# Performance work log

Measured on AMD Instinct MI355X. Metric: run time of the kernel, lower is better.

The kernel has to match this reference:

```python
import jax, jax.numpy as jnp
import numpy as np

C_Z = 128
N_HEADS = 4
HEAD_DIM = 32
TOTAL = N_HEADS * HEAD_DIM
B, N = 1, 256


def setup_inputs() -> dict:
    key = jax.random.key(0)
    ks = jax.random.split(key, 10)
    s = lambda k, sh: jax.random.normal(k, sh, dtype=jnp.float32) * 0.02
    return {
        "pair_representation": jax.random.normal(ks[0], (B, N, N, C_Z), dtype=jnp.float32),
        "ln_gamma": jnp.ones((C_Z,), jnp.float32),
        "ln_beta": jnp.zeros((C_Z,), jnp.float32),
        "Wq": s(ks[1], (C_Z, TOTAL)),
        "Wk": s(ks[2], (C_Z, TOTAL)),
        "Wv": s(ks[3], (C_Z, TOTAL)),
        "Wb": s(ks[4], (C_Z, N_HEADS)),
        "Wg": s(ks[5], (C_Z, TOTAL)),
        "bg": jnp.zeros((TOTAL,), jnp.float32),
        "Wo": s(ks[6], (TOTAL, C_Z)),
        "bo": jnp.zeros((C_Z,), jnp.float32),
    }


def reference(pair_representation, ln_gamma, ln_beta, Wq, Wk, Wv, Wb, Wg, bg, Wo, bo):
    x = pair_representation
    # LayerNorm over c_z
    mu = jnp.mean(x, axis=-1, keepdims=True)
    var = jnp.mean((x - mu) ** 2, axis=-1, keepdims=True)
    x = (x - mu) * jax.lax.rsqrt(var + 1e-5) * ln_gamma + ln_beta

    b, n, _, _ = x.shape
    split = lambda t: t.reshape(b, n, n, N_HEADS, HEAD_DIM)
    Q = split(x @ Wq)  # [b,i,j,h,d]
    K = split(x @ Wk)
    V = split(x @ Wv)
    G = jax.nn.sigmoid(split(x @ Wg + bg))
    Bias = x @ Wb  # [b,j,k,h]

    scores = jnp.einsum("bijhd,bikhd->bijkh", Q, K) / np.float32(np.sqrt(HEAD_DIM))
    scores = scores + Bias[:, None]  # broadcast over i
    attn = jax.nn.softmax(scores, axis=3)  # over k
    vals = jnp.einsum("bijkh,bikhd->bijhd", attn, V)
    vals = (G * vals).reshape(b, n, n, TOTAL)
    return vals @ Wo + bo
```

## Files before the change

kernel.cpp:

```cpp
#include <hip/hip_runtime.h>
#include <hip/hip_bf16.h>


#define QSCALE 0.17677669529663687f

typedef __attribute__((ext_vector_type(8))) short bf16x8;
typedef __attribute__((ext_vector_type(4))) float f32x4;

__device__ __forceinline__ ushort f2bf(float f) {
    uint32_t u = __builtin_bit_cast(uint32_t, f);
    uint32_t r = (u + 0x7FFFu + ((u >> 16) & 1u)) >> 16;
    return (ushort)r;
}
__device__ __forceinline__ float bf2f(ushort b) {
    return __builtin_bit_cast(float, ((uint32_t)b) << 16);
}
__device__ __forceinline__ uint pk2(float a, float b) {
    union { __hip_bfloat162 h; uint u; } cv;
    cv.h = __float22bfloat162_rn(make_float2(a, b));
    return cv.u;
}
__device__ __forceinline__ float4 ld4f(const float* p) { return *(const float4*)p; }

__global__ __launch_bounds__(256) void prep_kernel(
    const float* __restrict__ Wq, const float* __restrict__ Wk, const float* __restrict__ Wv,
    const float* __restrict__ Wb, const float* __restrict__ Wg, const float* __restrict__ Wo,
    ushort* __restrict__ Wfrag, ushort* __restrict__ WoFrag)
{
    int idx = blockIdx.x * 256 + threadIdx.x;
    if (idx < 67584) {
        int j = idx & 7, lane = (idx >> 3) & 63, ks = (idx >> 9) & 3, ct = idx >> 11;
        int n = ct * 16 + (lane & 15);
        int k = ks * 32 + (lane >> 4) * 8 + j;
        float v = 0.f;
        if (n < 128)      v = Wq[k * 128 + n] * QSCALE;
        else if (n < 256) v = Wk[k * 128 + (n - 128)];
        else if (n < 384) v = Wv[k * 128 + (n - 256)];
        else if (n < 512) v = Wg[k * 128 + (n - 384)];
        else if (n < 516) v = Wb[k * 4 + (n - 512)];
        Wfrag[idx] = f2bf(v);
    } else {
        int idx2 = idx - 67584;
        int j = idx2 & 7, lane = (idx2 >> 3) & 63, ks = (idx2 >> 9) & 3, ct = idx2 >> 11;
        int n = ct * 16 + (lane & 15);
        int k = ks * 32 + (lane >> 4) * 8 + j;
        WoFrag[idx2] = f2bf(Wo[k * 128 + n]);
    }
}

__global__ __launch_bounds__(256) void proj_kernel(
    const float* __restrict__ x, const float* __restrict__ gamma, const float* __restrict__ beta,
    const ushort* __restrict__ Wfrag, const float* __restrict__ bg,
    ushort* __restrict__ Qg, ushort* __restrict__ Kg, ushort* __restrict__ Vtg,
    ushort* __restrict__ Gg, float* __restrict__ BbF)
{
    __shared__ ushort Bs[11 * 2048];
    const int t = threadIdx.x;
    const int wave = t >> 6, lane = t & 63, m = lane & 15, quad = lane >> 4;
    const int p0 = blockIdx.x * 64;
    const int arow = p0 + wave * 16 + m;

    float4 xa[4][2];
    float sum = 0.f, ssq = 0.f;
#pragma unroll
    for (int ks = 0; ks < 4; ++ks) {
        const float* rp = x + arow * 128 + ks * 32 + quad * 8;
        xa[ks][0] = ld4f(rp);
        xa[ks][1] = ld4f(rp + 4);
#pragma unroll
        for (int q4 = 0; q4 < 2; ++q4) {
            float4 v = xa[ks][q4];
            sum += v.x + v.y + v.z + v.w;
            ssq += v.x * v.x + v.y * v.y + v.z * v.z + v.w * v.w;
        }
    }
    sum += __shfl_xor(sum, 16); ssq += __shfl_xor(ssq, 16);
    sum += __shfl_xor(sum, 32); ssq += __shfl_xor(ssq, 32);
    const float mu   = sum * (1.f / 128.f);
    const float var  = ssq * (1.f / 128.f) - mu * mu;
    const float rstd = rsqrtf(var + 1e-5f);

    bf16x8 xf[4];
#pragma unroll
    for (int ks = 0; ks < 4; ++ks) {
        union { bf16x8 v; uint u[4]; } xu;
#pragma unroll
        for (int q4 = 0; q4 < 2; ++q4) {
            const int c = ks * 32 + quad * 8 + q4 * 4;
            float4 g4 = ld4f(gamma + c);
            float4 b4 = ld4f(beta + c);
            float4 v = xa[ks][q4];
            float n0 = (v.x - mu) * rstd * g4.x + b4.x;
            float n1 = (v.y - mu) * rstd * g4.y + b4.y;
            float n2 = (v.z - mu) * rstd * g4.z + b4.z;
            float n3 = (v.w - mu) * rstd * g4.w + b4.w;
            xu.u[q4 * 2]     = pk2(n0, n1);
            xu.u[q4 * 2 + 1] = pk2(n2, n3);
        }
        xf[ks] = xu.v;
    }

    const int p = arow;
    const int i = p >> 8, j2 = p & 255;

    for (int phase = 0; phase < 3; ++phase) {
        const int ctbase = phase * 11;
        __syncthreads();
        const uint4* src = (const uint4*)(Wfrag + ctbase * 2048);
        uint4* dst = (uint4*)Bs;
#pragma unroll
        for (int r = 0; r < 11; ++r) dst[r * 256 + t] = src[r * 256 + t];
        __syncthreads();

        for (int ctl = 0; ctl < 11; ++ctl) {
            const int ct = ctbase + ctl;
            f32x4 acc = (f32x4){0.f, 0.f, 0.f, 0.f};
#pragma unroll
            for (int ks = 0; ks < 4; ++ks) {
                bf16x8 wfr = ((const bf16x8*)Bs)[(ctl * 4 + ks) * 64 + lane];
                acc = __builtin_amdgcn_mfma_f32_16x16x32_bf16(wfr, xf[ks], acc, 0, 0, 0);
            }
            if (ct < 32) {
                const int cls = ct >> 3;
                const int npb = (ct & 7) * 16 + quad * 4;
                const int hh = npb >> 5, d0 = npb & 31;
                if (cls == 2) {
                    const int vb = ((i * 4 + hh) * 32 + d0) * 256 + j2;
#pragma unroll
                    for (int r = 0; r < 4; ++r)
                        Vtg[vb + r * 256] = f2bf(acc[r]);
                } else {
                    const int off = ((i * 4 + hh) * 256 + j2) * 32 + d0;
                    uint2 u;
                    if (cls == 3) {
                        float4 bg4 = ld4f(&bg[npb]);
                        float z0 = 1.f / (1.f + __expf(-(acc[0] + bg4.x)));
                        float z1 = 1.f / (1.f + __expf(-(acc[1] + bg4.y)));
                        float z2 = 1.f / (1.f + __expf(-(acc[2] + bg4.z)));
                        float z3 = 1.f / (1.f + __expf(-(acc[3] + bg4.w)));
                        u.x = pk2(z0, z1); u.y = pk2(z2, z3);
                        *(uint2*)(&Gg[off]) = u;
                    } else {
                        u.x = pk2(acc[0], acc[1]); u.y = pk2(acc[2], acc[3]);
                        if (cls == 0) *(uint2*)(&Qg[off]) = u;
                        else          *(uint2*)(&Kg[off]) = u;
                    }
                }
            } else if (quad == 0) {
#pragma unroll
                for (int r = 0; r < 4; ++r) {
                    int addr = (((r * 16 + (i >> 4)) * 16 + (j2 >> 4)) * 64 +
                                ((j2 & 15) >> 2) * 16 + (i & 15)) * 4 + (j2 & 3);
                    BbF[addr] = acc[r];
                }
            }
        }
    }
}

__global__ __launch_bounds__(256) void attn_kernel(
    const ushort* __restrict__ Qg, const ushort* __restrict__ Kg, const ushort* __restrict__ Vtg,
    const ushort* __restrict__ Gg, const float* __restrict__ BbF, ushort* __restrict__ gvals)
{
    __shared__ ushort Pl[4][64 * 72];
    const int t = threadIdx.x;
    const int wave = t >> 6, lane = t & 63, m = lane & 15, quad = lane >> 4;
    const int ih = blockIdx.x, i = ih >> 2, h = ih & 3;

    const int j0 = wave * 64;
    bf16x8 qf[4];
#pragma unroll
    for (int jt = 0; jt < 4; ++jt)
        qf[jt] = *(const bf16x8*)(Qg + ih * 8192 + (j0 + jt * 16 + m) * 32 + quad * 8);

    f32x4 O[4][2];
    float lsum[4];
#pragma unroll
    for (int jt = 0; jt < 4; ++jt) {
        O[jt][0] = (f32x4){0.f, 0.f, 0.f, 0.f};
        O[jt][1] = (f32x4){0.f, 0.f, 0.f, 0.f};
        lsum[jt] = 0.f;
    }

    for (int kt2 = 0; kt2 < 4; ++kt2) {
        const int k0 = kt2 * 64;
        bf16x8 kf[4];
#pragma unroll
        for (int kk = 0; kk < 4; ++kk)
            kf[kk] = *(const bf16x8*)(Kg + ih * 8192 + (k0 + kk * 16 + m) * 32 + quad * 8);

#pragma unroll
        for (int jt = 0; jt < 4; ++jt) {
            const int jtg = wave * 4 + jt;
#pragma unroll
            for (int kk = 0; kk < 4; ++kk) {
                const int ktg = kt2 * 4 + kk;
                f32x4 bias = *(const f32x4*)(BbF + (((h * 16 + jtg) * 16 + ktg) * 64 + lane) * 4);
                f32x4 S = __builtin_amdgcn_mfma_f32_16x16x32_bf16(kf[kk], qf[jt], bias, 0, 0, 0);
                float pv0 = __expf(S[0]);
                float pv1 = __expf(S[1]);
                float pv2 = __expf(S[2]);
                float pv3 = __expf(S[3]);
                lsum[jt] += pv0 + pv1 + pv2 + pv3;
                uint2 u; u.x = pk2(pv0, pv1); u.y = pk2(pv2, pv3);
                *(uint2*)(&Pl[wave][(jt * 16 + m) * 72 + kk * 16 + quad * 4]) = u;
            }
        }
#pragma unroll
        for (int kc = 0; kc < 2; ++kc) {
            bf16x8 pf[4], vf[2];
#pragma unroll
            for (int jt = 0; jt < 4; ++jt)
                pf[jt] = *(const bf16x8*)(&Pl[wave][(jt * 16 + m) * 72 + kc * 32 + quad * 8]);
#pragma unroll
            for (int dt = 0; dt < 2; ++dt)
                vf[dt] = *(const bf16x8*)(Vtg + (ih * 32 + dt * 16 + m) * 256 + k0 + kc * 32 + quad * 8);
#pragma unroll
            for (int jt = 0; jt < 4; ++jt)
#pragma unroll
                for (int dt = 0; dt < 2; ++dt)
                    O[jt][dt] = __builtin_amdgcn_mfma_f32_16x16x32_bf16(
                        vf[dt], pf[jt], O[jt][dt], 0, 0, 0);
        }
    }

#pragma unroll
    for (int jt = 0; jt < 4; ++jt) {
        float s = lsum[jt];
        s += __shfl_xor(s, 16);
        s += __shfl_xor(s, 32);
        lsum[jt] = 1.f / s;
    }

#pragma unroll
    for (int jt = 0; jt < 4; ++jt) {
        const int j = j0 + jt * 16 + m;
        const float rl = lsum[jt];
#pragma unroll
        for (int dt = 0; dt < 2; ++dt) {
            const int d0 = dt * 16 + quad * 4;
            ushort4 gv = *(const ushort4*)(&Gg[ih * 8192 + j * 32 + d0]);
            float v0 = O[jt][dt][0] * rl * bf2f(gv.x);
            float v1 = O[jt][dt][1] * rl * bf2f(gv.y);
            float v2 = O[jt][dt][2] * rl * bf2f(gv.z);
            float v3 = O[jt][dt][3] * rl * bf2f(gv.w);
            uint2 u; u.x = pk2(v0, v1); u.y = pk2(v2, v3);
            *(uint2*)(&gvals[(i * 256 + j) * 128 + h * 32 + d0]) = u;
        }
    }
}

__global__ __launch_bounds__(256) void oproj_kernel(
    const ushort* __restrict__ gvals, const ushort* __restrict__ WoFrag,
    const float* __restrict__ bo, float* __restrict__ out)
{
    __shared__ ushort Bs[8 * 2048];
    const int t = threadIdx.x;
    const int wave = t >> 6, lane = t & 63, m = lane & 15, quad = lane >> 4;
    const int p0 = blockIdx.x * 64;
    {
        const uint4* src = (const uint4*)WoFrag;
        uint4* dst = (uint4*)Bs;
#pragma unroll
        for (int r = 0; r < 8; ++r) dst[r * 256 + t] = src[r * 256 + t];
    }
    bf16x8 gf[4];
    const int p = p0 + wave * 16 + m;
#pragma unroll
    for (int ks = 0; ks < 4; ++ks)
        gf[ks] = *(const bf16x8*)(gvals + p * 128 + ks * 32 + quad * 8);
    __syncthreads();

#pragma unroll
    for (int ct = 0; ct < 8; ++ct) {
        f32x4 acc = (f32x4){0.f, 0.f, 0.f, 0.f};
#pragma unroll
        for (int ks = 0; ks < 4; ++ks) {
            bf16x8 wfr = ((const bf16x8*)Bs)[(ct * 4 + ks) * 64 + lane];
            acc = __builtin_amdgcn_mfma_f32_16x16x32_bf16(wfr, gf[ks], acc, 0, 0, 0);
        }
        const int c0 = ct * 16 + quad * 4;
        float4 bov = ld4f(&bo[c0]);
        float4 v = make_float4(acc[0] + bov.x, acc[1] + bov.y,
                               acc[2] + bov.z, acc[3] + bov.w);
        *(float4*)(&out[p * 128 + c0]) = v;
    }
}

extern "C" void kernel_launch(void* const* d_in, const int* in_sizes, int n_in,
                              void* d_out, int out_size, void* d_ws, size_t ws_size,
                              hipStream_t stream) {
    const float* x     = (const float*)d_in[0];
    const float* gamma = (const float*)d_in[1];
    const float* beta  = (const float*)d_in[2];
    const float* Wq    = (const float*)d_in[3];
    const float* Wk    = (const float*)d_in[4];
    const float* Wv    = (const float*)d_in[5];
    const float* Wb    = (const float*)d_in[6];
    const float* Wg    = (const float*)d_in[7];
    const float* bg    = (const float*)d_in[8];
    const float* Wo    = (const float*)d_in[9];
    const float* bo    = (const float*)d_in[10];

    ushort* ws     = (ushort*)d_ws;
    ushort* Wfrag  = ws;
    ushort* WoFrag = Wfrag + 67584;
    ushort* Qg     = WoFrag + 16384;
    ushort* Kg     = Qg + 8388608;
    ushort* Vtg    = Kg + 8388608;
    ushort* Gg     = Vtg + 8388608;
    ushort* gvals  = Gg + 8388608;
    float*  BbF    = (float*)(gvals + 8388608);

    prep_kernel<<<328, 256, 0, stream>>>(Wq, Wk, Wv, Wb, Wg, Wo, Wfrag, WoFrag);
    proj_kernel<<<1024, 256, 0, stream>>>(x, gamma, beta, Wfrag, bg, Qg, Kg, Vtg, Gg, BbF);
    attn_kernel<<<1024, 256, 0, stream>>>(Qg, Kg, Vtg, Gg, BbF, gvals);
    oproj_kernel<<<1024, 256, 0, stream>>>(gvals, WoFrag, bo, (float*)d_out);
}
```

Before: 173.4 us.

## Fuse Q/K/V/G projections into attention kernel, precompute LayerNorm and bias

The LayerNorm output is now written once as bf16, and the pair bias is computed in a combined prep kernel. The separate projection and attention kernels are merged into one fused kernel per (i, head). It computes Q, K and V^T into shared memory, runs the attention with 16-wide k steps using 16x16x16 MFMA for PV, and recomputes the gate in the epilogue. This removes the large global round-trips for Q, K, Vt and G, in exchange for redundant projection work per head block and more LDS and register pressure.

New measurement: 172.6 us. About the same (-0.5%).

```diff
diff --git a/kernel.cpp b/kernel.cpp
--- a/kernel.cpp
+++ b/kernel.cpp
@@ -5,173 +5,239 @@
 #define QSCALE 0.17677669529663687f
 
 typedef __attribute__((ext_vector_type(8))) short bf16x8;
+typedef __attribute__((ext_vector_type(4))) short bf16x4;
 typedef __attribute__((ext_vector_type(4))) float f32x4;
+
+#define MFMA32(a, b, c) __builtin_amdgcn_mfma_f32_16x16x32_bf16((a), (b), (c), 0, 0, 0)
+
+__device__ __forceinline__ f32x4 mfma16_asm(bf16x4 a, bf16x4 b, f32x4 c) {
+    f32x4 d;
+    asm volatile("v_mfma_f32_16x16x16_bf16 %0, %1, %2, %3"
+                 : "=v"(d) : "v"(a), "v"(b), "v"(c));
+    return d;
+}
+
+#if !defined(__HIP_DEVICE_COMPILE__)
+#define MFMA16(a, b, c) (c)
+#elif __has_builtin(__builtin_amdgcn_mfma_f32_16x16x16bf16_1k)
+#define MFMA16(a, b, c) __builtin_amdgcn_mfma_f32_16x16x16bf16_1k((a), (b), (c), 0, 0, 0)
+#else
+#define MFMA16(a, b, c) mfma16_asm((a), (b), (c))
+#endif
 
 __device__ __forceinline__ ushort f2bf(float f) {
     uint32_t u = __builtin_bit_cast(uint32_t, f);
     uint32_t r = (u + 0x7FFFu + ((u >> 16) & 1u)) >> 16;
     return (ushort)r;
 }
-__device__ __forceinline__ float bf2f(ushort b) {
-    return __builtin_bit_cast(float, ((uint32_t)b) << 16);
-}
 __device__ __forceinline__ uint pk2(float a, float b) {
     union { __hip_bfloat162 h; uint u; } cv;
     cv.h = __float22bfloat162_rn(make_float2(a, b));
     return cv.u;
 }
-__device__ __forceinline__ float4 ld4f(const float* p) { return *(const float4*)p; }
-
-__global__ __launch_bounds__(256) void prep_kernel(
+
+__global__ __launch_bounds__(256) void prep_bias_kernel(
     const float* __restrict__ Wq, const float* __restrict__ Wk, const float* __restrict__ Wv,
-    const float* __restrict__ Wb, const float* __restrict__ Wg, const float* __restrict__ Wo,
-    ushort* __restrict__ Wfrag, ushort* __restrict__ WoFrag)
+    const float* __restrict__ Wg, const float* __restrict__ Wo, const float* __restrict__ Wb,
+    const float* __restrict__ x, const float* __restrict__ gamma, const float* __restrict__ beta,
+    ushort* __restrict__ Wfrag, ushort* __restrict__ WoFrag,
+    ushort* __restrict__ xn, float* __restrict__ BbF)
 {
-    int idx = blockIdx.x * 256 + threadIdx.x;
-    if (idx < 67584) {
-        int j = idx & 7, lane = (idx >> 3) & 63, ks = (idx >> 9) & 3, ct = idx >> 11;
-        int n = ct * 16 + (lane & 15);
-        int k = ks * 32 + (lane >> 4) * 8 + j;
-        float v = 0.f;
-        if (n < 128)      v = Wq[k * 128 + n] * QSCALE;
-        else if (n < 256) v = Wk[k * 128 + (n - 128)];
-        else if (n < 384) v = Wv[k * 128 + (n - 256)];
-        else if (n < 512) v = Wg[k * 128 + (n - 384)];
-        else if (n < 516) v = Wb[k * 4 + (n - 512)];
-        Wfrag[idx] = f2bf(v);
-    } else {
-        int idx2 = idx - 67584;
-        int j = idx2 & 7, lane = (idx2 >> 3) & 63, ks = (idx2 >> 9) & 3, ct = idx2 >> 11;
-        int n = ct * 16 + (lane & 15);
-        int k = ks * 32 + (lane >> 4) * 8 + j;
-        WoFrag[idx2] = f2bf(Wo[k * 128 + n]);
-    }
-}
-
-__global__ __launch_bounds__(256) void proj_kernel(
-    const float* __restrict__ x, const float* __restrict__ gamma, const float* __restrict__ beta,
-    const ushort* __restrict__ Wfrag, const float* __restrict__ bg,
-    ushort* __restrict__ Qg, ushort* __restrict__ Kg, ushort* __restrict__ Vtg,
-    ushort* __restrict__ Gg, float* __restrict__ BbF)
-{
-    __shared__ ushort Bs[11 * 2048];
+    __shared__ float WbS[512];
+    __shared__ float gS[128];
+    __shared__ float bS[128];
+
+    if (blockIdx.x < 320) {
+        int idx = blockIdx.x * 256 + threadIdx.x;
+        if (idx < 65536) {
+            int j = idx & 7, lane = (idx >> 3) & 63, ks = (idx >> 9) & 3, ct = idx >> 11;
+            int n = ct * 16 + (lane & 15);
+            int k = ks * 32 + (lane >> 4) * 8 + j;
+            float v;
+            if (n < 128)      v = Wq[k * 128 + n] * QSCALE;
+            else if (n < 256) v = Wk[k * 128 + (n - 128)];
+            else if (n < 384) v = Wv[k * 128 + (n - 256)];
+            else              v = Wg[k * 128 + (n - 384)];
+            Wfrag[idx] = f2bf(v);
+        } else {
+            int idx2 = idx - 65536;
+            int j = idx2 & 7, lane = (idx2 >> 3) & 63, ks = (idx2 >> 9) & 3, ct = idx2 >> 11;
+            int n = ct * 16 + (lane & 15);
+            int k = ks * 32 + (lane >> 4) * 8 + j;
+            WoFrag[idx2] = f2bf(Wo[k * 128 + n]);
+        }
+        return;
+    }
+
     const int t = threadIdx.x;
+    if (t < 128)      { *(f32x4*)&WbS[t * 4] = *(const f32x4*)(Wb + t * 4); }
+    else if (t < 160) { int c = (t - 128) * 4; *(f32x4*)&gS[c] = *(const f32x4*)(gamma + c); }
+    else if (t < 192) { int c = (t - 160) * 4; *(f32x4*)&bS[c] = *(const f32x4*)(beta + c); }
+    __syncthreads();
+
     const int wave = t >> 6, lane = t & 63, m = lane & 15, quad = lane >> 4;
-    const int p0 = blockIdx.x * 64;
-    const int arow = p0 + wave * 16 + m;
-
-    float4 xa[4][2];
+    const int p = (blockIdx.x - 320) * 64 + wave * 16 + m;
+
+    const float* rp0 = x + (size_t)p * 128;
+    f32x4 xa[4][2];
     float sum = 0.f, ssq = 0.f;
 #pragma unroll
     for (int ks = 0; ks < 4; ++ks) {
-        const float* rp = x + arow * 128 + ks * 32 + quad * 8;
-        xa[ks][0] = ld4f(rp);
-        xa[ks][1] = ld4f(rp + 4);
+        xa[ks][0] = *(const f32x4*)(rp0 + ks * 32 + quad * 8);
+        xa[ks][1] = *(const f32x4*)(rp0 + ks * 32 + quad * 8 + 4);
 #pragma unroll
         for (int q4 = 0; q4 < 2; ++q4) {
-            float4 v = xa[ks][q4];
-            sum += v.x + v.y + v.z + v.w;
-            ssq += v.x * v.x + v.y * v.y + v.z * v.z + v.w * v.w;
+            f32x4 v = xa[ks][q4];
+            sum += v[0] + v[1] + v[2] + v[3];
+            ssq += v[0]*v[0] + v[1]*v[1] + v[2]*v[2] + v[3]*v[3];
         }
     }
     sum += __shfl_xor(sum, 16); ssq += __shfl_xor(ssq, 16);
     sum += __shfl_xor(sum, 32); ssq += __shfl_xor(ssq, 32);
     const float mu   = sum * (1.f / 128.f);
-    const float var  = ssq * (1.f / 128.f) - mu * mu;
-    const float rstd = rsqrtf(var + 1e-5f);
-
-    bf16x8 xf[4];
+    const float rstd = rsqrtf(ssq * (1.f / 128.f) - mu * mu + 1e-5f);
+
+    float b0 = 0.f, b1 = 0.f, b2 = 0.f, b3 = 0.f;
 #pragma unroll
     for (int ks = 0; ks < 4; ++ks) {
-        union { bf16x8 v; uint u[4]; } xu;
+        uint4 pkd;
+        uint pw[4];
 #pragma unroll
         for (int q4 = 0; q4 < 2; ++q4) {
             const int c = ks * 32 + quad * 8 + q4 * 4;
-            float4 g4 = ld4f(gamma + c);
-            float4 b4 = ld4f(beta + c);
-            float4 v = xa[ks][q4];
-            float n0 = (v.x - mu) * rstd * g4.x + b4.x;
-            float n1 = (v.y - mu) * rstd * g4.y + b4.y;
-            float n2 = (v.z - mu) * rstd * g4.z + b4.z;
-            float n3 = (v.w - mu) * rstd * g4.w + b4.w;
-            xu.u[q4 * 2]     = pk2(n0, n1);
-            xu.u[q4 * 2 + 1] = pk2(n2, n3);
-        }
-        xf[ks] = xu.v;
-    }
-
-    const int p = arow;
-    const int i = p >> 8, j2 = p & 255;
-
-    for (int phase = 0; phase < 3; ++phase) {
-        const int ctbase = phase * 11;
-        __syncthreads();
-        const uint4* src = (const uint4*)(Wfrag + ctbase * 2048);
-        uint4* dst = (uint4*)Bs;
-#pragma unroll
-        for (int r = 0; r < 11; ++r) dst[r * 256 + t] = src[r * 256 + t];
-        __syncthreads();
-
-        for (int ctl = 0; ctl < 11; ++ctl) {
-            const int ct = ctbase + ctl;
-            f32x4 acc = (f32x4){0.f, 0.f, 0.f, 0.f};
-#pragma unroll
-            for (int ks = 0; ks < 4; ++ks) {
-                bf16x8 wfr = ((const bf16x8*)Bs)[(ctl * 4 + ks) * 64 + lane];
-                acc = __builtin_amdgcn_mfma_f32_16x16x32_bf16(wfr, xf[ks], acc, 0, 0, 0);
+            f32x4 v = xa[ks][q4];
+            float n0 = (v[0] - mu) * rstd * gS[c + 0] + bS[c + 0];
+            float n1 = (v[1] - mu) * rstd * gS[c + 1] + bS[c + 1];
+            float n2 = (v[2] - mu) * rstd * gS[c + 2] + bS[c + 2];
+            float n3 = (v[3] - mu) * rstd * gS[c + 3] + bS[c + 3];
+            pw[q4 * 2]     = pk2(n0, n1);
+            pw[q4 * 2 + 1] = pk2(n2, n3);
+            f32x4 w0 = *(const f32x4*)&WbS[(c + 0) * 4];
+            f32x4 w1 = *(const f32x4*)&WbS[(c + 1) * 4];
+            f32x4 w2 = *(const f32x4*)&WbS[(c + 2) * 4];
+            f32x4 w3 = *(const f32x4*)&WbS[(c + 3) * 4];
+            b0 += n0*w0[0] + n1*w1[0] + n2*w2[0] + n3*w3[0];
+            b1 += n0*w0[1] + n1*w1[1] + n2*w2[1] + n3*w3[1];
+            b2 += n0*w0[2] + n1*w1[2] + n2*w2[2] + n3*w3[2];
+            b3 += n0*w0[3] + n1*w1[3] + n2*w2[3] + n3*w3[3];
+        }
+        pkd.x = pw[0]; pkd.y = pw[1]; pkd.z = pw[2]; pkd.w = pw[3];
+        *(uint4*)(xn + (size_t)p * 128 + ks * 32 + quad * 8) = pkd;
+    }
+    b0 += __shfl_xor(b0, 16); b1 += __shfl_xor(b1, 16); b2 += __shfl_xor(b2, 16); b3 += __shfl_xor(b3, 16);
+    b0 += __shfl_xor(b0, 32); b1 += __shfl_xor(b1, 32); b2 += __shfl_xor(b2, 32); b3 += __shfl_xor(b3, 32);
+
+    if (quad == 0) {
+        const int row = p >> 8, col = p & 255;
+        float bb[4] = {b0, b1, b2, b3};
+#pragma unroll
+        for (int r = 0; r < 4; ++r) {
+            int addr = (((r * 16 + (row >> 4)) * 16 + (col >> 4)) * 64 +
+                        ((col & 15) >> 2) * 16 + (row & 15)) * 4 + (col & 3);
+            BbF[addr] = bb[r];
+        }
+    }
+}
+
+__global__ __launch_bounds__(256, 4) void fused_kernel(
+    const ushort* __restrict__ xn, const ushort* __restrict__ Wfrag,
+    const float* __restrict__ bg, const float* __restrict__ BbF,
+    ushort* __restrict__ gvals)
+{
+    __shared__ __align__(16) ushort SM[18688];
+    ushort* QK = SM;
+    ushort* VT = SM + 10240;
+
+    const int t = threadIdx.x;
+    const int w = t >> 6, lane = t & 63, m = lane & 15, quad = lane >> 4;
+    const int i = blockIdx.x >> 2, h = blockIdx.x & 3;
+    const ushort* xb = xn + ((size_t)i << 15);
+
+    {
+        const ushort* Wm = Wfrag + (0 + h * 2) * 2048;
+        bf16x8 wfr[2][4];
+#pragma unroll
+        for (int ctl = 0; ctl < 2; ++ctl)
+#pragma unroll
+            for (int ks = 0; ks < 4; ++ks)
+                wfr[ctl][ks] = *(const bf16x8*)(Wm + ctl * 2048 + ks * 512 + lane * 8);
+#pragma unroll
+        for (int grp = 0; grp < 4; ++grp) {
+            const int j = w * 64 + grp * 16 + m;
+            bf16x8 xg[4];
+            const ushort* xp = xb + (size_t)j * 128 + quad * 8;
+#pragma unroll
+            for (int ks = 0; ks < 4; ++ks) xg[ks] = *(const bf16x8*)(xp + ks * 32);
+#pragma unroll
+            for (int ctl = 0; ctl < 2; ++ctl) {
+                f32x4 acc = (f32x4){0.f, 0.f, 0.f, 0.f};
+#pragma unroll
+                for (int ks = 0; ks < 4; ++ks) acc = MFMA32(wfr[ctl][ks], xg[ks], acc);
+                uint2 u; u.x = pk2(acc[0], acc[1]); u.y = pk2(acc[2], acc[3]);
+                *(uint2*)(QK + j * 40 + ctl * 16 + quad * 4) = u;
             }
-            if (ct < 32) {
-                const int cls = ct >> 3;
-                const int npb = (ct & 7) * 16 + quad * 4;
-                const int hh = npb >> 5, d0 = npb & 31;
-                if (cls == 2) {
-                    const int vb = ((i * 4 + hh) * 32 + d0) * 256 + j2;
-#pragma unroll
-                    for (int r = 0; r < 4; ++r)
-                        Vtg[vb + r * 256] = f2bf(acc[r]);
-                } else {
-                    const int off = ((i * 4 + hh) * 256 + j2) * 32 + d0;
-                    uint2 u;
-                    if (cls == 3) {
-                        float4 bg4 = ld4f(&bg[npb]);
-                        float z0 = 1.f / (1.f + __expf(-(acc[0] + bg4.x)));
-                        float z1 = 1.f / (1.f + __expf(-(acc[1] + bg4.y)));
-                        float z2 = 1.f / (1.f + __expf(-(acc[2] + bg4.z)));
-                        float z3 = 1.f / (1.f + __expf(-(acc[3] + bg4.w)));
-                        u.x = pk2(z0, z1); u.y = pk2(z2, z3);
-                        *(uint2*)(&Gg[off]) = u;
-                    } else {
-                        u.x = pk2(acc[0], acc[1]); u.y = pk2(acc[2], acc[3]);
-                        if (cls == 0) *(uint2*)(&Qg[off]) = u;
-                        else          *(uint2*)(&Kg[off]) = u;
-                    }
-                }
-            } else if (quad == 0) {
-#pragma unroll
-                for (int r = 0; r < 4; ++r) {
-                    int addr = (((r * 16 + (i >> 4)) * 16 + (j2 >> 4)) * 64 +
-                                ((j2 & 15) >> 2) * 16 + (i & 15)) * 4 + (j2 & 3);
-                    BbF[addr] = acc[r];
-                }
+        }
+    }
+    bf16x8 qf[4];
+#pragma unroll
+    for (int jt = 0; jt < 4; ++jt)
+        qf[jt] = *(const bf16x8*)(QK + (w * 64 + jt * 16 + m) * 40 + quad * 8);
+    asm volatile("" ::: "memory");
+
+    {
+        const ushort* Wm = Wfrag + (8 + h * 2) * 2048;
+        bf16x8 wfr[2][4];
+#pragma unroll
+        for (int ctl = 0; ctl < 2; ++ctl)
+#pragma unroll
+            for (int ks = 0; ks < 4; ++ks)
+                wfr[ctl][ks] = *(const bf16x8*)(Wm + ctl * 2048 + ks * 512 + lane * 8);
+#pragma unroll
+        for (int grp = 0; grp < 4; ++grp) {
+            const int k = w * 64 + grp * 16 + m;
+            bf16x8 xg[4];
+            const ushort* xp = xb + (size_t)k * 128 + quad * 8;
+#pragma unroll
+            for (int ks = 0; ks < 4; ++ks) xg[ks] = *(const bf16x8*)(xp + ks * 32);
+#pragma unroll
+            for (int ctl = 0; ctl < 2; ++ctl) {
+                f32x4 acc = (f32x4){0.f, 0.f, 0.f, 0.f};
+#pragma unroll
+                for (int ks = 0; ks < 4; ++ks) acc = MFMA32(wfr[ctl][ks], xg[ks], acc);
+                uint2 u; u.x = pk2(acc[0], acc[1]); u.y = pk2(acc[2], acc[3]);
+                *(uint2*)(QK + k * 40 + ctl * 16 + quad * 4) = u;
             }
         }
     }
-}
-
-__global__ __launch_bounds__(256) void attn_kernel(
-    const ushort* __restrict__ Qg, const ushort* __restrict__ Kg, const ushort* __restrict__ Vtg,
-    const ushort* __restrict__ Gg, const float* __restrict__ BbF, ushort* __restrict__ gvals)
-{
-    __shared__ ushort Pl[4][64 * 72];
-    const int t = threadIdx.x;
-    const int wave = t >> 6, lane = t & 63, m = lane & 15, quad = lane >> 4;
-    const int ih = blockIdx.x, i = ih >> 2, h = ih & 3;
-
-    const int j0 = wave * 64;
-    bf16x8 qf[4];
-#pragma unroll
-    for (int jt = 0; jt < 4; ++jt)
-        qf[jt] = *(const bf16x8*)(Qg + ih * 8192 + (j0 + jt * 16 + m) * 32 + quad * 8);
+    asm volatile("" ::: "memory");
+
+    {
+        const ushort* Wm = Wfrag + (16 + h * 2) * 2048;
+        bf16x8 wfr[2][4];
+#pragma unroll
+        for (int ctl = 0; ctl < 2; ++ctl)
+#pragma unroll
+            for (int ks = 0; ks < 4; ++ks)
+                wfr[ctl][ks] = *(const bf16x8*)(Wm + ctl * 2048 + ks * 512 + lane * 8);
+#pragma unroll
+        for (int grp = 0; grp < 4; ++grp) {
+            const int k = w * 64 + grp * 16 + m;
+            bf16x8 xg[4];
+            const ushort* xp = xb + (size_t)k * 128 + quad * 8;
+#pragma unroll
+            for (int ks = 0; ks < 4; ++ks) xg[ks] = *(const bf16x8*)(xp + ks * 32);
+#pragma unroll
+            for (int ctl = 0; ctl < 2; ++ctl) {
+                f32x4 acc = (f32x4){0.f, 0.f, 0.f, 0.f};
+#pragma unroll
+                for (int ks = 0; ks < 4; ++ks) acc = MFMA32(wfr[ctl][ks], xg[ks], acc);
+#pragma unroll
+                for (int r = 0; r < 4; ++r)
+                    VT[(ctl * 16 + quad * 4 + r) * 264 + k] = f2bf(acc[r]);
+            }
+        }
+    }
+    __syncthreads();
 
     f32x4 O[4][2];
     float lsum[4];
@@ -181,46 +247,28 @@
         O[jt][1] = (f32x4){0.f, 0.f, 0.f, 0.f};
         lsum[jt] = 0.f;
     }
-
-    for (int kt2 = 0; kt2 < 4; ++kt2) {
-        const int k0 = kt2 * 64;
-        bf16x8 kf[4];
-#pragma unroll
-        for (int kk = 0; kk < 4; ++kk)
-            kf[kk] = *(const bf16x8*)(Kg + ih * 8192 + (k0 + kk * 16 + m) * 32 + quad * 8);
-
+    const float* bb = BbF + ((size_t)(h * 16 + w * 4) << 12) + (lane << 2);
+
+    for (int kh = 0; kh < 16; ++kh) {
+        bf16x8 kf = *(const bf16x8*)(QK + (kh * 16 + m) * 40 + quad * 8);
+        bf16x4 vf[2];
+#pragma unroll
+        for (int dt = 0; dt < 2; ++dt) {
+            uint2 vv = *(const uint2*)(VT + (dt * 16 + m) * 264 + kh * 16 + quad * 4);
+            vf[dt] = __builtin_bit_cast(bf16x4, vv);
+        }
 #pragma unroll
         for (int jt = 0; jt < 4; ++jt) {
-            const int jtg = wave * 4 + jt;
-#pragma unroll
-            for (int kk = 0; kk < 4; ++kk) {
-                const int ktg = kt2 * 4 + kk;
-                f32x4 bias = *(const f32x4*)(BbF + (((h * 16 + jtg) * 16 + ktg) * 64 + lane) * 4);
-                f32x4 S = __builtin_amdgcn_mfma_f32_16x16x32_bf16(kf[kk], qf[jt], bias, 0, 0, 0);
-                float pv0 = __expf(S[0]);
-                float pv1 = __expf(S[1]);
-                float pv2 = __expf(S[2]);
-                float pv3 = __expf(S[3]);
-                lsum[jt] += pv0 + pv1 + pv2 + pv3;
-                uint2 u; u.x = pk2(pv0, pv1); u.y = pk2(pv2, pv3);
-                *(uint2*)(&Pl[wave][(jt * 16 + m) * 72 + kk * 16 + quad * 4]) = u;
-            }
-        }
-#pragma unroll
-        for (int kc = 0; kc < 2; ++kc) {
-            bf16x8 pf[4], vf[2];
-#pragma unroll
-            for (int jt = 0; jt < 4; ++jt)
-                pf[jt] = *(const bf16x8*)(&Pl[wave][(jt * 16 + m) * 72 + kc * 32 + quad * 8]);
+            f32x4 S = *(const f32x4*)(bb + (jt << 12) + (kh << 8));
+            S = MFMA32(kf, qf[jt], S);
+            float p0 = __expf(S[0]), p1 = __expf(S[1]);
+            float p2 = __expf(S[2]), p3 = __expf(S[3]);
+            lsum[jt] += p0 + p1 + p2 + p3;
+            uint2 pu; pu.x = pk2(p0, p1); pu.y = pk2(p2, p3);
+            bf16x4 pf = __builtin_bit_cast(bf16x4, pu);
 #pragma unroll
             for (int dt = 0; dt < 2; ++dt)
-                vf[dt] = *(const bf16x8*)(Vtg + (ih * 32 + dt * 16 + m) * 256 + k0 + kc * 32 + quad * 8);
-#pragma unroll
-            for (int jt = 0; jt < 4; ++jt)
-#pragma unroll
-                for (int dt = 0; dt < 2; ++dt)
-                    O[jt][dt] = __builtin_amdgcn_mfma_f32_16x16x32_bf16(
-                        vf[dt], pf[jt], O[jt][dt], 0, 0, 0);
+                O[jt][dt] = MFMA16(vf[dt], pf, O[jt][dt]);
         }
     }
 
@@ -232,20 +280,41 @@
         lsum[jt] = 1.f / s;
     }
 
-#pragma unroll
-    for (int jt = 0; jt < 4; ++jt) {
-        const int j = j0 + jt * 16 + m;
-        const float rl = lsum[jt];
-#pragma unroll
-        for (int dt = 0; dt < 2; ++dt) {
-            const int d0 = dt * 16 + quad * 4;
-            ushort4 gv = *(const ushort4*)(&Gg[ih * 8192 + j * 32 + d0]);
-            float v0 = O[jt][dt][0] * rl * bf2f(gv.x);
-            float v1 = O[jt][dt][1] * rl * bf2f(gv.y);
-            float v2 = O[jt][dt][2] * rl * bf2f(gv.z);
-            float v3 = O[jt][dt][3] * rl * bf2f(gv.w);
-            uint2 u; u.x = pk2(v0, v1); u.y = pk2(v2, v3);
-            *(uint2*)(&gvals[(i * 256 + j) * 128 + h * 32 + d0]) = u;
+    {
+        const ushort* Wm = Wfrag + (24 + h * 2) * 2048;
+        bf16x8 wfr[2][4];
+        f32x4 bg4[2];
+#pragma unroll
+        for (int ctl = 0; ctl < 2; ++ctl) {
+#pragma unroll
+            for (int ks = 0; ks < 4; ++ks)
+                wfr[ctl][ks] = *(const bf16x8*)(Wm + ctl * 2048 + ks * 512 + lane * 8);
+            bg4[ctl] = *(const f32x4*)(bg + h * 32 + ctl * 16 + quad * 4);
+        }
+#pragma unroll
+        for (int grp = 0; grp < 4; ++grp) {
+            const int j = w * 64 + grp * 16 + m;
+            const float rl = lsum[grp];
+            bf16x8 xg[4];
+            const ushort* xp = xb + (size_t)j * 128 + quad * 8;
+#pragma unroll
+            for (int ks = 0; ks < 4; ++ks) xg[ks] = *(const bf16x8*)(xp + ks * 32);
+#pragma unroll
+            for (int ctl = 0; ctl < 2; ++ctl) {
+                f32x4 acc = (f32x4){0.f, 0.f, 0.f, 0.f};
+#pragma unroll
+                for (int ks = 0; ks < 4; ++ks) acc = MFMA32(wfr[ctl][ks], xg[ks], acc);
+                float g0 = 1.f / (1.f + __expf(-(acc[0] + bg4[ctl][0])));
+                float g1 = 1.f / (1.f + __expf(-(acc[1] + bg4[ctl][1])));
+                float g2 = 1.f / (1.f + __expf(-(acc[2] + bg4[ctl][2])));
+                float g3 = 1.f / (1.f + __expf(-(acc[3] + bg4[ctl][3])));
+                float v0 = O[grp][ctl][0] * rl * g0;
+                float v1 = O[grp][ctl][1] * rl * g1;
+                float v2 = O[grp][ctl][2] * rl * g2;
+                float v3 = O[grp][ctl][3] * rl * g3;
+                uint2 u; u.x = pk2(v0, v1); u.y = pk2(v2, v3);
+                *(uint2*)(gvals + (size_t)(i * 256 + j) * 128 + h * 32 + ctl * 16 + quad * 4) = u;
+            }
         }
     }
 }
@@ -268,7 +337,7 @@
     const int p = p0 + wave * 16 + m;
 #pragma unroll
     for (int ks = 0; ks < 4; ++ks)
-        gf[ks] = *(const bf16x8*)(gvals + p * 128 + ks * 32 + quad * 8);
+        gf[ks] = *(const bf16x8*)(gvals + (size_t)p * 128 + ks * 32 + quad * 8);
     __syncthreads();
 
 #pragma unroll
@@ -277,13 +346,13 @@
 #pragma unroll
         for (int ks = 0; ks < 4; ++ks) {
             bf16x8 wfr = ((const bf16x8*)Bs)[(ct * 4 + ks) * 64 + lane];
-            acc = __builtin_amdgcn_mfma_f32_16x16x32_bf16(wfr, gf[ks], acc, 0, 0, 0);
+            acc = MFMA32(wfr, gf[ks], acc);
         }
         const int c0 = ct * 16 + quad * 4;
-        float4 bov = ld4f(&bo[c0]);
-        float4 v = make_float4(acc[0] + bov.x, acc[1] + bov.y,
-                               acc[2] + bov.z, acc[3] + bov.w);
-        *(float4*)(&out[p * 128 + c0]) = v;
+        f32x4 bov = *(const f32x4*)(bo + c0);
+        float4 v = make_float4(acc[0] + bov[0], acc[1] + bov[1],
+                               acc[2] + bov[2], acc[3] + bov[3]);
+        *(float4*)(&out[(size_t)p * 128 + c0]) = v;
     }
 }
 
@@ -302,18 +371,16 @@
     const float* Wo    = (const float*)d_in[9];
     const float* bo    = (const float*)d_in[10];
 
-    ushort* ws     = (ushort*)d_ws;
-    ushort* Wfrag  = ws;
-    ushort* WoFrag = Wfrag + 67584;
-    ushort* Qg     = WoFrag + 16384;
-    ushort* Kg     = Qg + 8388608;
-    ushort* Vtg    = Kg + 8388608;
-    ushort* Gg     = Vtg + 8388608;
-    ushort* gvals  = Gg + 8388608;
-    float*  BbF    = (float*)(gvals + 8388608);
-
-    prep_kernel<<<328, 256, 0, stream>>>(Wq, Wk, Wv, Wb, Wg, Wo, Wfrag, WoFrag);
-    proj_kernel<<<1024, 256, 0, stream>>>(x, gamma, beta, Wfrag, bg, Qg, Kg, Vtg, Gg, BbF);
-    attn_kernel<<<1024, 256, 0, stream>>>(Qg, Kg, Vtg, Gg, BbF, gvals);
-    oproj_kernel<<<1024, 256, 0, stream>>>(gvals, WoFrag, bo, (float*)d_out);
-}
+    ushort* ws      = (ushort*)d_ws;
+    ushort* Wfrag   = ws;
+    ushort* WoFragp = ws + 65536;
+    ushort* xn      = ws + 81920;
+    ushort* gvals   = ws + 81920 + 8388608;
+    float*  BbF     = (float*)(ws + 81920 + 2 * 8388608);
+
+    prep_bias_kernel<<<1344, 256, 0, stream>>>(Wq, Wk, Wv, Wg, Wo, Wb,
+                                               x, gamma, beta,
+                                               Wfrag, WoFragp, xn, BbF);
+    fused_kernel<<<1024, 256, 0, stream>>>(xn, Wfrag, bg, BbF, gvals);
+    oproj_kernel<<<1024, 256, 0, stream>>>(gvals, WoFragp, bo, (float*)d_out);
+}
```
